# Kernel tuning notes

Measured on AMD Instinct MI355X. Metric: run time of the kernel, lower is better.

## Reference

```python
import jax, jax.numpy as jnp
import numpy as np

BLOCK_SIZE = 32
FORMAT_MAX = 1.0
MANTISSA_BITS = 3.0   # E4M3-like element quantization
CYCLE_BUDGET = 16.0   # B_final: MSD cycle budget per output channel
ONLINE_DELAY = 2.0    # delta: online multiplier startup delay
NEG_LOG2 = -60.0


def _safe_log2(x):
    # log2 mapping 0 / negative to a large negative number
    return jnp.where(x > 0, jnp.log2(jnp.maximum(x, 1e-45)), NEG_LOG2)


def _quantize_elements(xn):
    # round-to-nearest float with MANTISSA_BITS mantissa bits (values in [-1, 1])
    a = jnp.abs(xn)
    e = jnp.floor(_safe_log2(a))
    step = jnp.exp2(e - MANTISSA_BITS)
    return jnp.where(a > 0, jnp.round(xn / step) * step, 0.0)


def _quantize_to_blocks(x_blocks, eps=1e-30):
    # x_blocks: (..., nb, bs) -> (x_q same shape, scales (..., nb))
    max_abs = jnp.max(jnp.abs(x_blocks), axis=-1)
    scales = jnp.maximum(max_abs / FORMAT_MAX, eps)
    x_q = _quantize_elements(x_blocks / scales[..., None])
    return x_q, scales


def _compute_inter_block_delays(w_scales, x_scales):
    # w_scales: (out, nb), x_scales: (N, nb)
    combined_log2 = _safe_log2(x_scales)[:, None, :] + _safe_log2(w_scales)[None, :, :]
    combined_e = jnp.floor(combined_log2)                 # (N, out, nb)
    e_max = jnp.max(combined_e, axis=-1)                  # (N, out)
    return e_max[..., None] - combined_e, e_max


def _compute_intra_block_delays(x_q_blocks):
    # x_q_blocks: (N, nb, bs)
    abs_vals = jnp.abs(x_q_blocks)
    elem_log2 = jnp.where(abs_vals > 0,
                          jnp.floor(jnp.log2(jnp.maximum(abs_vals, 1e-45))),
                          NEG_LOG2)
    e_max_block = jnp.max(elem_log2, axis=-1, keepdims=True)
    return e_max_block - elem_log2


def _msd_truncate(value, num_digits):
    # keep the `num_digits` most-significant NAF (non-adjacent form) digits
    abs_v = jnp.abs(value)
    sign = jnp.sign(value)
    mask = (num_digits > 0) & (abs_v > 0)
    msb_pos = jnp.floor(jnp.log2(jnp.maximum(abs_v, 1e-45)))
    scale_up = jnp.exp2(jnp.clip(23.0 - msb_pos, -126.0, 126.0))
    x_scaled = jnp.round(abs_v * scale_up).astype(jnp.int32)   # ~2^23..2^24
    x_h = x_scaled >> 1
    s = x_scaled + x_h
    naf_pos = s & ~x_h
    naf_neg = x_h & ~s
    combined = naf_pos | naf_neg
    naf_width = jnp.where(
        combined > 0,
        jnp.floor(jnp.log2(jnp.maximum(combined.astype(jnp.float32), 1.0))).astype(jnp.int32) + 1,
        jnp.zeros_like(combined))
    drop = jnp.clip(naf_width - num_digits.astype(jnp.int32), 0, 31)
    keep_mask = ~((jnp.int32(1) << drop) - 1)
    recon = ((naf_pos & keep_mask).astype(jnp.float32)
             - (naf_neg & keep_mask).astype(jnp.float32)) / scale_up
    return jnp.where(mask, sign * recon, 0.0)


def setup_inputs() -> dict:
    key = jax.random.key(0)
    k1, k2, k3 = jax.random.split(key, 3)
    N, in_f, out_f = 128, 1024, 512
    x = jax.random.normal(k1, (N, in_f), dtype=jnp.float32)
    weight = jax.random.normal(k2, (out_f, in_f), dtype=jnp.float32) * 0.02
    bias = jax.random.normal(k3, (out_f,), dtype=jnp.float32) * 0.01
    return {"x": x, "weight": weight, "bias": bias}


def reference(x, weight, bias):
    N, in_f = x.shape
    out_f = weight.shape[0]
    nb = in_f // BLOCK_SIZE
    xb = x.reshape(N, nb, BLOCK_SIZE)
    wb = weight.reshape(out_f, nb, BLOCK_SIZE)
    x_q, x_s = _quantize_to_blocks(xb)   # (N, nb, bs), (N, nb)
    w_q, w_s = _quantize_to_blocks(wb)   # (out, nb, bs), (out, nb)
    inter, e_max = _compute_inter_block_delays(w_s, x_s)  # (N, out, nb)
    intra = _compute_intra_block_delays(x_q)              # (N, nb, bs)
    # effective NAF digit budget per product element
    eff = (CYCLE_BUDGET - ONLINE_DELAY) - inter[..., None] - intra[:, None, :, :]
    prod = x_q[:, None, :, :] * w_q[None, :, :, :]        # (N, out, nb, bs)
    trunc = jax.lax.stop_gradient(_msd_truncate(prod, eff))  # torch.no_grad
    block_dots = jnp.sum(trunc, axis=-1)                  # (N, out, nb)
    out = jnp.einsum('nb,ob,nob->no', x_s, w_s, block_dots) + bias
    return out
```

## Files before the change

### kernel.cpp

```cpp
#include <hip/hip_runtime.h>
#include <cstdint>


#define NN 128
#define KF 1024
#define OF 512
#define NB 32
#define KS 16


__global__ __launch_bounds__(256) void prep_kernel(
    const float* __restrict__ x, const float* __restrict__ w,
    uint2* __restrict__ xaP2, uint2* __restrict__ wB,
    float* __restrict__ lxT, float* __restrict__ lw) {
  int bid = blockIdx.x;
  int tid = (int)threadIdx.x;
  bool is_x = bid < 512;
  int eid = is_x ? bid * 256 + tid : (bid - 512) * 256 + tid;
  float v = is_x ? x[eid] : w[eid];
  float a = fabsf(v);
  float m = a;
  #pragma unroll
  for (int s = 1; s < 32; s <<= 1) m = fmaxf(m, __shfl_xor(m, s, 32));
  float scale = fmaxf(m, 1e-30f);
  float xn = v / scale;
  unsigned nb_ = __float_as_uint(xn);
  unsigned ab = nb_ & 0x7fffffffu;
  bool zz = ab < 0x00800000u;
  int e = (int)(ab >> 23) - 127;
  float am = __uint_as_float((ab & 0x007fffffu) | 0x3f800000u);
  int mi = (int)rintf(am * 8.0f);
  if (mi == 16) { mi = 8; ++e; }
  if (zz) mi = 0;
  unsigned sgn = nb_ & 0x80000000u;
  unsigned sb = __float_as_uint(scale);
  if (is_x) {
    int ei = zz ? -1000000 : e;
    int em = ei;
    #pragma unroll
    for (int s = 1; s < 32; s <<= 1) em = max(em, __shfl_xor(em, s, 32));
    int di = zz ? 63 : min(em - e, 63);
    unsigned fb = zz ? 0u : ((sb + (((unsigned)e) << 23)) | sgn);
    unsigned meta = (unsigned)mi | ((unsigned)di << 8);
    int k = eid & 1023, n = eid >> 10;
    xaP2[((k >> 1) * NN + n) * 2 + (k & 1)] = make_uint2(fb, meta);
    if ((tid & 31) == 0) lxT[(k >> 5) * NN + n] = log2f(scale);
  } else {
    unsigned fb = zz ? 0u : ((sb + (((unsigned)(e - 7)) << 23)) | sgn);
    wB[eid] = make_uint2(fb, (unsigned)mi);
    int o = eid >> 10, k = eid & 1023;
    if ((tid & 31) == 0) lw[o * NB + (k >> 5)] = log2f(scale);
  }
}

__global__ __launch_bounds__(256) void emax_kernel(
    const float* __restrict__ lxT, const float* __restrict__ lw,
    float* __restrict__ emaxT) {
  int gid = blockIdx.x * 256 + (int)threadIdx.x;
  int n = gid & (NN - 1), o = gid >> 7;
  float m = -1e30f;
  #pragma unroll
  for (int b = 0; b < NB; ++b)
    m = fmaxf(m, floorf(lxT[b * NN + n] + lw[o * NB + b]));
  emaxT[o * NN + n] = m;
}

__device__ __forceinline__ void prod_acc(int mx, int di, float fxs,
                                         unsigned fwbits, int mw, int nb,
                                         float& acc) {
  int p  = __mul24(mx, mw);
  int s3 = (p << 1) + p;
  int cx = s3 ^ p;
  int wd = 32 - __clz(cx);
  int u  = wd + di + nb;
  int drop = min(max(u, 0), wd);
  unsigned keep = 0xFFFFFFFFu << drop;
  unsigned kc = keep & (unsigned)cx;
  int r = (int)((unsigned)s3 & kc) - (int)((unsigned)p & kc);
  acc = fmaf((float)r * fxs, __uint_as_float(fwbits), acc);
}

__global__ __launch_bounds__(256, 4) void main_kernel(
    const uint4* __restrict__ xaP, const uint2* __restrict__ wB,
    const float* __restrict__ lxT, const float* __restrict__ lw,
    const float* __restrict__ emaxT, float* __restrict__ part) {
  __shared__ __align__(16) uint2 tile[16 * 64 + 2];
  int bid = blockIdx.x;
  int s   = bid & 15;
  int og  = (bid >> 4) & 31;
  int ng  = bid >> 9;
  int tid = (int)threadIdx.x, lane = tid & 63, w4 = tid >> 6;
  int o_base = og * 16;
  int k0 = s * 64;
  int n = ng * 64 + lane;
  int b0 = s * 2;

  {
    int r = tid >> 4, c = tid & 15;
    const uint4* src = reinterpret_cast<const uint4*>(&wB[(o_base + r) * KF + k0]);
    uint4* dst = reinterpret_cast<uint4*>(&tile[r * 64]);
    dst[c] = src[c];
    dst[c + 16] = src[c + 16];
  }

  int ow = o_base + w4 * 4;
  float lx0 = lxT[b0 * NN + n];
  float lx1 = lxT[(b0 + 1) * NN + n];
  int nbA[4], nbB[4];
  #pragma unroll
  for (int j = 0; j < 4; ++j) {
    float em = emaxT[(ow + j) * NN + n];
    nbA[j] = -(int)(14.0f - em + floorf(lx0 + lw[(ow + j) * NB + b0]));
    nbB[j] = -(int)(14.0f - em + floorf(lx1 + lw[(ow + j) * NB + b0 + 1]));
  }
  __syncthreads();

  const uint4* xaRow = &xaP[(size_t)(k0 >> 1) * NN + n];
#define LDT(j, g) (*reinterpret_cast<const uint4*>(&tile[(w4 * 4 + (j)) * 64 + 2 * (g)]))
  float acc0 = 0.f, acc1 = 0.f, acc2 = 0.f, acc3 = 0.f;

#define COMPUTE(gv, xv, t0, t1, t2, t3)                                    \
  {                                                                        \
    int mx0 = (int)(xv.y & 255u), di0 = (int)(xv.y >> 8);                  \
    int mx1 = (int)(xv.w & 255u), di1 = (int)(xv.w >> 8);                  \
    float fx0 = __uint_as_float(xv.x), fx1 = __uint_as_float(xv.z);        \
    int nb0 = (gv) < 16 ? nbA[0] : nbB[0];                                 \
    int nb1 = (gv) < 16 ? nbA[1] : nbB[1];                                 \
    int nb2 = (gv) < 16 ? nbA[2] : nbB[2];                                 \
    int nb3 = (gv) < 16 ? nbA[3] : nbB[3];                                 \
    prod_acc(mx0, di0, fx0, t0.x, (int)t0.y, nb0, acc0);                   \
    prod_acc(mx1, di1, fx1, t0.z, (int)t0.w, nb0, acc0);                   \
    prod_acc(mx0, di0, fx0, t1.x, (int)t1.y, nb1, acc1);                   \
    prod_acc(mx1, di1, fx1, t1.z, (int)t1.w, nb1, acc1);                   \
    prod_acc(mx0, di0, fx0, t2.x, (int)t2.y, nb2, acc2);                   \
    prod_acc(mx1, di1, fx1, t2.z, (int)t2.w, nb2, acc2);                   \
    prod_acc(mx0, di0, fx0, t3.x, (int)t3.y, nb3, acc3);                   \
    prod_acc(mx1, di1, fx1, t3.z, (int)t3.w, nb3, acc3);                   \
  }

  uint4 xa_ = xaRow[0];
  uint4 ta0 = LDT(0, 0), ta1 = LDT(1, 0), ta2 = LDT(2, 0), ta3 = LDT(3, 0);

  #pragma unroll 1
  for (int g2 = 0; g2 < 16; ++g2) {
    int gb = 2 * g2 + 1;
    uint4 xb_ = xaRow[(size_t)gb * NN];
    uint4 tb0 = LDT(0, gb), tb1 = LDT(1, gb), tb2 = LDT(2, gb), tb3 = LDT(3, gb);
    COMPUTE(2 * g2, xa_, ta0, ta1, ta2, ta3);
    int gc = gb + 1;
    xa_ = xaRow[(size_t)gc * NN];
    ta0 = LDT(0, gc); ta1 = LDT(1, gc); ta2 = LDT(2, gc); ta3 = LDT(3, gc);
    COMPUTE(gb, xb_, tb0, tb1, tb2, tb3);
  }

  float* ps = &part[((size_t)(s * OF) + ow) * NN + n];
  ps[0 * NN] = acc0;
  ps[1 * NN] = acc1;
  ps[2 * NN] = acc2;
  ps[3 * NN] = acc3;
#undef COMPUTE
#undef LDT
}

__global__ __launch_bounds__(256) void reduce_kernel(
    const float* __restrict__ part, const float* __restrict__ bias,
    float* __restrict__ out) {
  int gid = blockIdx.x * 256 + (int)threadIdx.x;
  int n = gid & (NN - 1), o = gid >> 7;
  float sum = bias[o];
  #pragma unroll
  for (int c = 0; c < KS; ++c) sum += part[((size_t)c * OF + o) * NN + n];
  out[n * OF + o] = sum;
}

extern "C" void kernel_launch(void* const* d_in, const int* in_sizes, int n_in,
                              void* d_out, int out_size, void* d_ws, size_t ws_size,
                              hipStream_t stream) {
  const float* x    = (const float*)d_in[0];
  const float* w    = (const float*)d_in[1];
  const float* bias = (const float*)d_in[2];
  float* out = (float*)d_out;
  char* ws = (char*)d_ws;
  uint2* xaP2  = (uint2*)(ws);
  uint4* xaP   = (uint4*)(ws);
  uint2* wB    = (uint2*)(ws + 1048576);
  float* lxT   = (float*)(ws + 5242880);
  float* lw    = (float*)(ws + 5259264);
  float* emaxT = (float*)(ws + 5324800);
  float* part  = (float*)(ws + 5580800);

  prep_kernel<<<2560, 256, 0, stream>>>(x, w, xaP2, wB, lxT, lw);
  emax_kernel<<<256, 256, 0, stream>>>(lxT, lw, emaxT);
  main_kernel<<<1024, 256, 0, stream>>>(xaP, wB, lxT, lw, emaxT, part);
  reduce_kernel<<<256, 256, 0, stream>>>(part, bias, out);
}
```

Measured before the change: 98.20 us.

## Retile main kernel to 8 outputs per wave with 32-way K split

Result: no change. 99.23 us (+1.0%).

```diff
diff --git a/kernel.cpp b/kernel.cpp
--- a/kernel.cpp
+++ b/kernel.cpp
@@ -6,7 +6,7 @@
 #define KF 1024
 #define OF 512
 #define NB 32
-#define KS 16
+#define KS 32
 
 
 __global__ __launch_bounds__(256) void prep_kernel(
@@ -35,11 +35,7 @@
   unsigned sgn = nb_ & 0x80000000u;
   unsigned sb = __float_as_uint(scale);
   if (is_x) {
-    int ei = zz ? -1000000 : e;
-    int em = ei;
-    #pragma unroll
-    for (int s = 1; s < 32; s <<= 1) em = max(em, __shfl_xor(em, s, 32));
-    int di = zz ? 63 : min(em - e, 63);
+    int di = zz ? 63 : min(-e, 63);
     unsigned fb = zz ? 0u : ((sb + (((unsigned)e) << 23)) | sgn);
     unsigned meta = (unsigned)mi | ((unsigned)di << 8);
     int k = eid & 1023, n = eid >> 10;
@@ -84,80 +80,72 @@
     const uint4* __restrict__ xaP, const uint2* __restrict__ wB,
     const float* __restrict__ lxT, const float* __restrict__ lw,
     const float* __restrict__ emaxT, float* __restrict__ part) {
-  __shared__ __align__(16) uint2 tile[16 * 64 + 2];
+  __shared__ __align__(16) uint2 tile[32 * 32 + 2];
   int bid = blockIdx.x;
-  int s   = bid & 15;
-  int og  = (bid >> 4) & 31;
+  int s   = bid & 31;
+  int og  = (bid >> 5) & 15;
   int ng  = bid >> 9;
   int tid = (int)threadIdx.x, lane = tid & 63, w4 = tid >> 6;
-  int o_base = og * 16;
-  int k0 = s * 64;
+  int o_base = og * 32;
+  int k0 = s * 32;
   int n = ng * 64 + lane;
-  int b0 = s * 2;
 
   {
-    int r = tid >> 4, c = tid & 15;
+    int r = tid >> 3, c = tid & 7;
     const uint4* src = reinterpret_cast<const uint4*>(&wB[(o_base + r) * KF + k0]);
-    uint4* dst = reinterpret_cast<uint4*>(&tile[r * 64]);
+    uint4* dst = reinterpret_cast<uint4*>(&tile[r * 32]);
     dst[c] = src[c];
-    dst[c + 16] = src[c + 16];
+    dst[c + 8] = src[c + 8];
   }
 
-  int ow = o_base + w4 * 4;
-  float lx0 = lxT[b0 * NN + n];
-  float lx1 = lxT[(b0 + 1) * NN + n];
-  int nbA[4], nbB[4];
+  int ow = o_base + w4 * 8;
+  float lxv = lxT[s * NN + n];
+  float acc[8];
+  int nbv[8];
   #pragma unroll
-  for (int j = 0; j < 4; ++j) {
+  for (int j = 0; j < 8; ++j) {
+    acc[j] = 0.f;
     float em = emaxT[(ow + j) * NN + n];
-    nbA[j] = -(int)(14.0f - em + floorf(lx0 + lw[(ow + j) * NB + b0]));
-    nbB[j] = -(int)(14.0f - em + floorf(lx1 + lw[(ow + j) * NB + b0 + 1]));
+    nbv[j] = -(int)(14.0f - em + floorf(lxv + lw[(ow + j) * NB + s]));
   }
   __syncthreads();
 
   const uint4* xaRow = &xaP[(size_t)(k0 >> 1) * NN + n];
-#define LDT(j, g) (*reinterpret_cast<const uint4*>(&tile[(w4 * 4 + (j)) * 64 + 2 * (g)]))
-  float acc0 = 0.f, acc1 = 0.f, acc2 = 0.f, acc3 = 0.f;
-
-#define COMPUTE(gv, xv, t0, t1, t2, t3)                                    \
+#define LDT(j, g) (*reinterpret_cast<const uint4*>(&tile[(w4 * 8 + (j)) * 32 + 2 * (g)]))
+#define COMPUTE(xv, T)                                                     \
   {                                                                        \
     int mx0 = (int)(xv.y & 255u), di0 = (int)(xv.y >> 8);                  \
     int mx1 = (int)(xv.w & 255u), di1 = (int)(xv.w >> 8);                  \
     float fx0 = __uint_as_float(xv.x), fx1 = __uint_as_float(xv.z);        \
-    int nb0 = (gv) < 16 ? nbA[0] : nbB[0];                                 \
-    int nb1 = (gv) < 16 ? nbA[1] : nbB[1];                                 \
-    int nb2 = (gv) < 16 ? nbA[2] : nbB[2];                                 \
-    int nb3 = (gv) < 16 ? nbA[3] : nbB[3];                                 \
-    prod_acc(mx0, di0, fx0, t0.x, (int)t0.y, nb0, acc0);                   \
-    prod_acc(mx1, di1, fx1, t0.z, (int)t0.w, nb0, acc0);                   \
-    prod_acc(mx0, di0, fx0, t1.x, (int)t1.y, nb1, acc1);                   \
-    prod_acc(mx1, di1, fx1, t1.z, (int)t1.w, nb1, acc1);                   \
-    prod_acc(mx0, di0, fx0, t2.x, (int)t2.y, nb2, acc2);                   \
-    prod_acc(mx1, di1, fx1, t2.z, (int)t2.w, nb2, acc2);                   \
-    prod_acc(mx0, di0, fx0, t3.x, (int)t3.y, nb3, acc3);                   \
-    prod_acc(mx1, di1, fx1, t3.z, (int)t3.w, nb3, acc3);                   \
+    _Pragma("unroll")                                                      \
+    for (int j = 0; j < 8; ++j) {                                          \
+      prod_acc(mx0, di0, fx0, T[j].x, (int)T[j].y, nbv[j], acc[j]);        \
+      prod_acc(mx1, di1, fx1, T[j].z, (int)T[j].w, nbv[j], acc[j]);        \
+    }                                                                      \
   }
 
   uint4 xa_ = xaRow[0];
-  uint4 ta0 = LDT(0, 0), ta1 = LDT(1, 0), ta2 = LDT(2, 0), ta3 = LDT(3, 0);
+  uint4 ta[8], tb[8];
+  #pragma unroll
+  for (int j = 0; j < 8; ++j) ta[j] = LDT(j, 0);
 
   #pragma unroll 1
-  for (int g2 = 0; g2 < 16; ++g2) {
+  for (int g2 = 0; g2 < 8; ++g2) {
     int gb = 2 * g2 + 1;
     uint4 xb_ = xaRow[(size_t)gb * NN];
-    uint4 tb0 = LDT(0, gb), tb1 = LDT(1, gb), tb2 = LDT(2, gb), tb3 = LDT(3, gb);
-    COMPUTE(2 * g2, xa_, ta0, ta1, ta2, ta3);
+    #pragma unroll
+    for (int j = 0; j < 8; ++j) tb[j] = LDT(j, gb);
+    COMPUTE(xa_, ta);
     int gc = gb + 1;
     xa_ = xaRow[(size_t)gc * NN];
-    ta0 = LDT(0, gc); ta1 = LDT(1, gc); ta2 = LDT(2, gc); ta3 = LDT(3, gc);
-    COMPUTE(gb, xb_, tb0, tb1, tb2, tb3);
+    #pragma unroll
+    for (int j = 0; j < 8; ++j) ta[j] = LDT(j, gc);
+    COMPUTE(xb_, tb);
   }
 
-  float* ps = &part[((size_t)(s * OF) + ow) * NN + n];
-  ps[0 * NN] = acc0;
-  ps[1 * NN] = acc1;
-  ps[2 * NN] = acc2;
-  ps[3 * NN] = acc3;
+  #pragma unroll
+  for (int j = 0; j < 8; ++j)
+    part[((size_t)(s * OF) + ow + j) * NN + n] = acc[j];
 #undef COMPUTE
 #undef LDT
 }
```
